# Kernel optimization log

Hardware: AMD Instinct MI355X
Metric: run time of the kernel (lower is better)

The kernel has to match this reference:

```python
import jax, jax.numpy as jnp
import numpy as np

B, N, DIM, H, DH = 32, 1024, 512, 8, 64
SCALE = DH ** -0.5


def setup_inputs() -> dict:
    key = jax.random.key(0)
    k1, k2, k3, k4 = jax.random.split(key, 4)
    x = jax.random.normal(k1, (B, N, DIM), dtype=jnp.float32)
    W_qkv = jax.random.normal(k2, (DIM, 3 * H * DH), dtype=jnp.float32) * (DIM ** -0.5)
    W_out = jax.random.normal(k3, (H * DH, DIM), dtype=jnp.float32) * ((H * DH) ** -0.5)
    b_out = jnp.zeros((DIM,), dtype=jnp.float32)
    decay_mask = jax.random.uniform(k4, (1, H, N, N), dtype=jnp.float32)
    return {"x": x, "W_qkv": W_qkv, "W_out": W_out, "b_out": b_out,
            "decay_mask": decay_mask}


def reference(x, W_qkv, W_out, b_out, decay_mask):
    b, n, _ = x.shape
    qkv = x @ W_qkv                                  # [b, n, 3*h*d]
    q, k, v = jnp.split(qkv, 3, axis=-1)
    reshape = lambda t: t.reshape(b, n, H, DH).transpose(0, 2, 1, 3)  # b h n d
    q, k, v = reshape(q), reshape(k), reshape(v)
    dots = jnp.einsum('bhid,bhjd->bhij', q, k) * SCALE
    attn = jax.nn.softmax(dots, axis=-1)
    attn = attn * decay_mask                          # post-softmax decay mask
    out = jnp.einsum('bhij,bhjd->bhid', attn, v)      # [b, h, n, d]
    out = out.transpose(0, 2, 1, 3).reshape(b, n, H * DH)
    return out @ W_out + b_out
```

## Files before the change

kernel.cpp:

```cpp
#include <hip/hip_runtime.h>
#include <hip/hip_fp16.h>
#include <math.h>

#define Bb 32
#define Nn 1024
#define DIMc 512
#define Hh 8
#define DHd 64
#define GK 512

typedef __attribute__((ext_vector_type(8))) short short8;
typedef __attribute__((ext_vector_type(8))) _Float16 half8;
typedef __attribute__((ext_vector_type(2))) __fp16 fp16x2;
typedef __attribute__((ext_vector_type(4))) float floatx4;

#define MFMA16 __builtin_amdgcn_mfma_f32_16x16x32_f16

#if __has_builtin(__builtin_amdgcn_exp2f)
#define EXP2(x) __builtin_amdgcn_exp2f(x)
#else
#define EXP2(x) __expf((x) * 0.6931471805599453f)
#endif

__device__ __forceinline__ unsigned short f16_bits(float f) {
    return __half_as_ushort(__float2half(f));
}
__device__ __forceinline__ int cvt_pk_f16(float a, float b) {
    fp16x2 r = __builtin_amdgcn_cvt_pkrtz(a, b);
    return __builtin_bit_cast(int, r);
}

__global__ __launch_bounds__(256) void transpose_half_kernel(
    const float* __restrict__ src, int K, int N,
    unsigned short* __restrict__ dh)
{
    __shared__ float T[32][33];
    const int tid = threadIdx.x;
    const int c = tid & 31, r0 = tid >> 5;
    const int nb = blockIdx.x * 32, kb = blockIdx.y * 32;
    #pragma unroll
    for (int i = 0; i < 4; ++i)
        T[r0 + i * 8][c] = src[(size_t)(kb + r0 + i * 8) * N + nb + c];
    __syncthreads();
    #pragma unroll
    for (int i = 0; i < 4; ++i) {
        int n = r0 + i * 8;
        dh[(size_t)(nb + n) * K + kb + c] = f16_bits(T[c][n]);
    }
}

__global__ __launch_bounds__(256) void decay_to_half_kernel(
    const float* __restrict__ D, unsigned short* __restrict__ D16)
{
    size_t i = ((size_t)blockIdx.x * 256 + threadIdx.x) * 4;
    float4 v = *(const float4*)(D + i);
    ushort4 o;
    o.x = f16_bits(v.x * 0.00390625f);
    o.y = f16_bits(v.y * 0.00390625f);
    o.z = f16_bits(v.z * 0.00390625f);
    o.w = f16_bits(v.w * 0.00390625f);
    *(ushort4*)(D16 + i) = o;
}

__global__ __launch_bounds__(256) void x_to_half_kernel(
    const float* __restrict__ X, unsigned short* __restrict__ Xf)
{
    size_t i = ((size_t)blockIdx.x * 256 + threadIdx.x) * 8;
    float4 a = *(const float4*)(X + i);
    float4 b = *(const float4*)(X + i + 4);
    float f[8] = {a.x, a.y, a.z, a.w, b.x, b.y, b.z, b.w};
    short8 o;
    #pragma unroll
    for (int e = 0; e < 8; ++e) o[e] = (short)f16_bits(f[e]);
    *(short8*)(Xf + i) = o;
}

__device__ __forceinline__ void gload_lds16(const unsigned short* g, unsigned short* l) {
    __builtin_amdgcn_global_load_lds(
        (const __attribute__((address_space(1))) unsigned int*)g,
        (__attribute__((address_space(3))) unsigned int*)l,
        16, 0, 0);
}

__global__ __launch_bounds__(256) void gemm_qkv_mfma(
    const unsigned short* __restrict__ Xf, const unsigned short* __restrict__ Wf,
    unsigned short* __restrict__ Qf, unsigned short* __restrict__ Kf,
    unsigned short* __restrict__ Vt)
{
    __shared__ union {
        struct { unsigned short Af[2][4096], Bf[2][4096]; } s;
        unsigned short bounce[128][136];
    } u;

    const int tid  = threadIdx.x;
    const int w    = tid >> 6;
    const int lane = tid & 63;
    const int quad = lane >> 4;
    const int l16  = lane & 15;
    const int lb = blockIdx.x;
    const int wg = (lb & 7) * 384 + (lb >> 3);
    const int n0 = (wg % 12) * 128;
    const int m0 = (wg / 12) * 128;
    const int wm = w >> 1, wn = w & 1;

    floatx4 acc[4][4];
    #pragma unroll
    for (int im = 0; im < 4; ++im)
        #pragma unroll
        for (int in = 0; in < 4; ++in)
            acc[im][in] = (floatx4){0.f, 0.f, 0.f, 0.f};

    #pragma unroll
    for (int i = 0; i < 2; ++i) {
        const int row = i * 64 + w * 16 + l16;
        const size_t aoff = (size_t)(m0 + row) * GK + quad * 8;
        const size_t boff = (size_t)(n0 + row) * GK + quad * 8;
        const int lbe = (i * 4 + w) * 512;
        gload_lds16(Xf + aoff, &u.s.Af[0][lbe]);
        gload_lds16(Wf + boff, &u.s.Bf[0][lbe]);
    }

    int cur = 0;
    for (int k0 = 0; k0 < GK; k0 += 32) {
        __syncthreads();
        if (k0 + 32 < GK) {
            const int kn = k0 + 32;
            #pragma unroll
            for (int i = 0; i < 2; ++i) {
                const int row = i * 64 + w * 16 + l16;
                const size_t aoff = (size_t)(m0 + row) * GK + kn + quad * 8;
                const size_t boff = (size_t)(n0 + row) * GK + kn + quad * 8;
                const int lbe = (i * 4 + w) * 512;
                gload_lds16(Xf + aoff, &u.s.Af[cur ^ 1][lbe]);
                gload_lds16(Wf + boff, &u.s.Bf[cur ^ 1][lbe]);
            }
        }

        half8 faf[4], fbf[4];
        #pragma unroll
        for (int t = 0; t < 4; ++t) {
            const int ca = ((wm * 4 + t) * 4 + quad) * 16 + l16;
            faf[t] = *(const half8*)&u.s.Af[cur][ca * 8];
            const int cb = ((wn * 4 + t) * 4 + quad) * 16 + l16;
            fbf[t] = *(const half8*)&u.s.Bf[cur][cb * 8];
        }
        #pragma unroll
        for (int im = 0; im < 4; ++im)
            #pragma unroll
            for (int in = 0; in < 4; ++in)
                acc[im][in] = MFMA16(faf[im], fbf[in], acc[im][in], 0, 0, 0);
        cur ^= 1;
    }

    const int which = n0 >> 9;
    const int b    = m0 >> 10;
    const int tokb = m0 & 1023;
    if (which < 2) {
        unsigned short* OUT = which ? Kf : Qf;
        const float sc = which ? 1.0f : 0.18033688011112042f;
        #pragma unroll
        for (int im = 0; im < 4; ++im) {
            const int tok = tokb + wm * 64 + im * 16 + quad * 4;
            #pragma unroll
            for (int in = 0; in < 4; ++in) {
                const int ncol = n0 + wn * 64 + in * 16 + l16;
                const int h = (ncol & 511) >> 6, d = ncol & 63;
                const size_t base = ((size_t)(b * Hh + h) * Nn + tok) * DHd + d;
                #pragma unroll
                for (int r = 0; r < 4; ++r)
                    OUT[base + (size_t)r * DHd] = f16_bits(acc[im][in][r] * sc);
            }
        }
    } else {
        __syncthreads();
        #pragma unroll
        for (int im = 0; im < 4; ++im)
            #pragma unroll
            for (int in = 0; in < 4; ++in)
                #pragma unroll
                for (int r = 0; r < 4; ++r)
                    u.bounce[wm * 64 + im * 16 + quad * 4 + r][wn * 64 + in * 16 + l16] =
                        f16_bits(acc[im][in][r]);
        __syncthreads();
        const int c = tid >> 1, tq = (tid & 1) * 64;
        const int h = ((n0 + c) & 511) >> 6, d = c & 63;
        unsigned short* vbase = Vt + ((size_t)(b * Hh + h) * DHd + d) * Nn + tokb;
        #pragma unroll
        for (int uu = 0; uu < 8; ++uu) {
            short8 v8;
            #pragma unroll
            for (int e = 0; e < 8; ++e)
                v8[e] = (short)u.bounce[tq + uu * 8 + e][c];
            *(short8*)&vbase[tq + uu * 8] = v8;
        }
    }
}

__global__ __launch_bounds__(256) void attn_mfma_kernel(
    const unsigned short* __restrict__ Qf, const unsigned short* __restrict__ Kf,
    const unsigned short* __restrict__ Vt, const unsigned short* __restrict__ D16,
    unsigned short* __restrict__ AOf)
{
    __shared__ unsigned short Kfs[2][32][72];
    __shared__ unsigned short Vts[2][64][40];

    const int tid  = threadIdx.x;
    const int wave = tid >> 6;
    const int lane = tid & 63;
    const int quad = lane >> 4;
    const int l16  = lane & 15;
    const int lb   = blockIdx.x;
    const int xcd  = lb & 7;
    const int r_   = lb >> 3;
    const int h    = r_ >> 5;
    const int rem  = r_ & 31;
    const int i0   = (rem >> 2) << 7;
    const int b    = xcd * 4 + (rem & 3);
    const int bh   = b * 8 + h;
    const int iw   = i0 + wave * 32;

    const size_t qoffA = ((size_t)bh * Nn + iw + l16) * DHd + quad * 8;
    const size_t qoffB = qoffA + (size_t)16 * DHd;
    const half8 qA0 = *(const half8*)(Qf + qoffA);
    const half8 qA1 = *(const half8*)(Qf + qoffA + 32);
    const half8 qB0 = *(const half8*)(Qf + qoffB);
    const half8 qB1 = *(const half8*)(Qf + qoffB + 32);

    floatx4 oA[4], oB[4];
    #pragma unroll
    for (int nt = 0; nt < 4; ++nt) {
        oA[nt] = (floatx4){0.f, 0.f, 0.f, 0.f};
        oB[nt] = (floatx4){0.f, 0.f, 0.f, 0.f};
    }
    float lA = 0.f, lB = 0.f;

    const int sj  = tid >> 3, sc2 = (tid & 7) * 8;
    const int prow = ((sj >> 2) & 1) * 16 + ((sj >> 3) << 2) + (sj & 3);
    const int vd  = tid >> 2, vj8 = (tid & 3) * 8;
    const unsigned short* DpA = D16 + ((size_t)h * Nn + iw + l16) * Nn + quad * 8;
    const unsigned short* DpB = DpA + (size_t)16 * Nn;

    const unsigned short* kpf = Kf + (size_t)bh * Nn * DHd + (size_t)sj * DHd + sc2;
    const unsigned short* vpv = Vt + (size_t)bh * DHd * Nn + (size_t)vd * Nn + vj8;

    short8 pk_f = *(const short8*)kpf; kpf += 32 * DHd;
    short8 pk_v = *(const short8*)vpv; vpv += 32;
    *(short8*)&Kfs[0][prow][sc2] = pk_f;
    *(short8*)&Vts[0][vd][vj8]   = pk_v;
    __syncthreads();

    int cur = 0;
    for (int j0 = 0; j0 < Nn; j0 += 32) {
        pk_f = *(const short8*)kpf; kpf += 32 * DHd;
        pk_v = *(const short8*)vpv; vpv += 32;
        const short8 dcA = *(const short8*)(DpA + j0);
        const short8 dcB = *(const short8*)(DpB + j0);

        floatx4 sA[2], sB[2];
        #pragma unroll
        for (int nh = 0; nh < 2; ++nh) {
            const int kr = nh * 16 + l16;
            half8 kf0 = *(const half8*)&Kfs[cur][kr][quad * 8];
            half8 kf1 = *(const half8*)&Kfs[cur][kr][32 + quad * 8];
            floatx4 a = (floatx4){0.f, 0.f, 0.f, 0.f};
            a = MFMA16(kf0, qA0, a, 0, 0, 0);
            a = MFMA16(kf1, qA1, a, 0, 0, 0);
            sA[nh] = a;
            floatx4 c = (floatx4){0.f, 0.f, 0.f, 0.f};
            c = MFMA16(kf0, qB0, c, 0, 0, 0);
            c = MFMA16(kf1, qB1, c, 0, 0, 0);
            sB[nh] = c;
        }

        float pA[8], pB[8];
        #pragma unroll
        for (int e = 0; e < 4; ++e) {
            pA[e]     = EXP2(sA[0][e]);
            pA[4 + e] = EXP2(sA[1][e]);
            pB[e]     = EXP2(sB[0][e]);
            pB[4 + e] = EXP2(sB[1][e]);
        }
        lA += ((pA[0] + pA[1]) + (pA[2] + pA[3])) + ((pA[4] + pA[5]) + (pA[6] + pA[7]));
        lB += ((pB[0] + pB[1]) + (pB[2] + pB[3])) + ((pB[4] + pB[5]) + (pB[6] + pB[7]));

        union { int i4[4]; half8 v8; } pfA, pfB;
        const int* dA = (const int*)&dcA;
        const int* dB = (const int*)&dcB;
        #pragma unroll
        for (int e = 0; e < 4; ++e) {
            fp16x2 pa = __builtin_bit_cast(fp16x2, cvt_pk_f16(pA[2 * e], pA[2 * e + 1]));
            fp16x2 da = __builtin_bit_cast(fp16x2, dA[e]);
            pfA.i4[e] = __builtin_bit_cast(int, pa * da);
            fp16x2 pb = __builtin_bit_cast(fp16x2, cvt_pk_f16(pB[2 * e], pB[2 * e + 1]));
            fp16x2 db = __builtin_bit_cast(fp16x2, dB[e]);
            pfB.i4[e] = __builtin_bit_cast(int, pb * db);
        }
        #pragma unroll
        for (int nt = 0; nt < 4; ++nt) {
            half8 vf = *(const half8*)&Vts[cur][nt * 16 + l16][quad * 8];
            oA[nt] = MFMA16(pfA.v8, vf, oA[nt], 0, 0, 0);
            oB[nt] = MFMA16(pfB.v8, vf, oB[nt], 0, 0, 0);
        }

        *(short8*)&Kfs[cur ^ 1][prow][sc2] = pk_f;
        *(short8*)&Vts[cur ^ 1][vd][vj8]   = pk_v;
        __syncthreads();
        cur ^= 1;
    }

    float lsA = lA;
    lsA += __shfl_xor(lsA, 16);
    lsA += __shfl_xor(lsA, 32);
    float lsB = lB;
    lsB += __shfl_xor(lsB, 16);
    lsB += __shfl_xor(lsB, 32);
    const float invA = 256.f / lsA;
    const float invB = 256.f / lsB;
    float irA[4], irB[4];
    #pragma unroll
    for (int r = 0; r < 4; ++r) {
        irA[r] = __shfl(invA, quad * 4 + r);
        irB[r] = __shfl(invB, quad * 4 + r);
    }
    const size_t aobA = ((size_t)b * Nn + iw) * DIMc + h * DHd;
    const size_t aobB = aobA + (size_t)16 * DIMc;
    #pragma unroll
    for (int nt = 0; nt < 4; ++nt)
        #pragma unroll
        for (int r = 0; r < 4; ++r) {
            const size_t ro = (size_t)(quad * 4 + r) * DIMc + nt * 16 + l16;
            AOf[aobA + ro] = f16_bits(oA[nt][r] * irA[r]);
            AOf[aobB + ro] = f16_bits(oB[nt][r] * irB[r]);
        }
}

__global__ __launch_bounds__(256) void gemm_out_mfma(
    const unsigned short* __restrict__ Af, const unsigned short* __restrict__ Wf,
    const float* __restrict__ bias, float* __restrict__ C)
{
    __shared__ struct { unsigned short Aa[2][4096], Bf[2][4096]; } s;

    const int tid  = threadIdx.x;
    const int w    = tid >> 6;
    const int lane = tid & 63;
    const int quad = lane >> 4;
    const int l16  = lane & 15;
    const int lb = blockIdx.x;
    const int wg = (lb & 7) * 128 + (lb >> 3);
    const int n0 = (wg & 3) * 128;
    const int m0 = (wg >> 2) * 128;
    const int wm = w >> 1, wn = w & 1;

    floatx4 acc[4][4];
    #pragma unroll
    for (int im = 0; im < 4; ++im)
        #pragma unroll
        for (int in = 0; in < 4; ++in)
            acc[im][in] = (floatx4){0.f, 0.f, 0.f, 0.f};

    #pragma unroll
    for (int i = 0; i < 2; ++i) {
        const int row = i * 64 + w * 16 + l16;
        const size_t aoff = (size_t)(m0 + row) * GK + quad * 8;
        const size_t boff = (size_t)(n0 + row) * GK + quad * 8;
        const int lbe = (i * 4 + w) * 512;
        gload_lds16(Af + aoff, &s.Aa[0][lbe]);
        gload_lds16(Wf + boff, &s.Bf[0][lbe]);
    }

    int cur = 0;
    for (int k0 = 0; k0 < GK; k0 += 32) {
        __syncthreads();
        if (k0 + 32 < GK) {
            const int kn = k0 + 32;
            #pragma unroll
            for (int i = 0; i < 2; ++i) {
                const int row = i * 64 + w * 16 + l16;
                const size_t aoff = (size_t)(m0 + row) * GK + kn + quad * 8;
                const size_t boff = (size_t)(n0 + row) * GK + kn + quad * 8;
                const int lbe = (i * 4 + w) * 512;
                gload_lds16(Af + aoff, &s.Aa[cur ^ 1][lbe]);
                gload_lds16(Wf + boff, &s.Bf[cur ^ 1][lbe]);
            }
        }

        half8 faf[4], fbf[4];
        #pragma unroll
        for (int t = 0; t < 4; ++t) {
            const int ca = ((wm * 4 + t) * 4 + quad) * 16 + l16;
            faf[t] = *(const half8*)&s.Aa[cur][ca * 8];
            const int cb = ((wn * 4 + t) * 4 + quad) * 16 + l16;
            fbf[t] = *(const half8*)&s.Bf[cur][cb * 8];
        }
        #pragma unroll
        for (int im = 0; im < 4; ++im)
            #pragma unroll
            for (int in = 0; in < 4; ++in)
                acc[im][in] = MFMA16(faf[im], fbf[in], acc[im][in], 0, 0, 0);
        cur ^= 1;
    }

    float biasv[4];
    #pragma unroll
    for (int in = 0; in < 4; ++in) biasv[in] = bias[n0 + wn * 64 + in * 16 + l16];
    #pragma unroll
    for (int im = 0; im < 4; ++im)
        #pragma unroll
        for (int in = 0; in < 4; ++in) {
            const int mrow = m0 + wm * 64 + im * 16 + quad * 4;
            const int ncol = n0 + wn * 64 + in * 16 + l16;
            #pragma unroll
            for (int r = 0; r < 4; ++r)
                C[(size_t)(mrow + r) * DIMc + ncol] = acc[im][in][r] + biasv[in];
        }
}

extern "C" void kernel_launch(void* const* d_in, const int* in_sizes, int n_in,
                              void* d_out, int out_size, void* d_ws, size_t ws_size,
                              hipStream_t stream)
{
    const float* x     = (const float*)d_in[0];
    const float* Wqkv  = (const float*)d_in[1];
    const float* Wout  = (const float*)d_in[2];
    const float* bout  = (const float*)d_in[3];
    const float* decay = (const float*)d_in[4];

    const size_t E = (size_t)32768 * 512;
    unsigned short* p = (unsigned short*)d_ws;
    unsigned short* Qf  = p; p += E;
    unsigned short* Kf  = p; p += E;
    unsigned short* Vt  = p; p += E;
    unsigned short* AOf = p; p += E;
    unsigned short* Wq  = p; p += 786432;
    unsigned short* Wo  = p; p += 262144;
    unsigned short* D16 = p;
    unsigned short* Xf = AOf;

    transpose_half_kernel<<<dim3(48, 16), 256, 0, stream>>>(Wqkv, 512, 1536, Wq);
    transpose_half_kernel<<<dim3(16, 16), 256, 0, stream>>>(Wout, 512, 512, Wo);
    decay_to_half_kernel<<<dim3(8192), 256, 0, stream>>>(decay, D16);
    x_to_half_kernel<<<dim3(8192), 256, 0, stream>>>(x, Xf);
    gemm_qkv_mfma<<<dim3(3072), 256, 0, stream>>>(Xf, Wq, Qf, Kf, Vt);
    attn_mfma_kernel<<<dim3(2048), 256, 0, stream>>>(Qf, Kf, Vt, D16, AOf);
    gemm_out_mfma<<<dim3(1024), 256, 0, stream>>>(AOf, Wo, bout, (float*)d_out);
}
```

Before: 288.1 us.

## Triple-buffer LDS staging in QKV and output GEMMs with explicit waitcnt

Both MFMA GEMM kernels now use three LDS stages instead of two and prefetch two k-tiles ahead. A manual `s_waitcnt vmcnt(4)` plus a raw barrier replaces `__syncthreads`, so the loads for the next tile stay in flight while the current tile is computed. The aim is to hide global-to-LDS latency better in the projection GEMMs. The cost is LDS rising from 32 KB to 48 KB per block, which can lower occupancy. The last iterations also issue unguarded prefetches past the K extent; their buffers are never read, but the final rows may read slightly beyond the array.

```diff
diff --git a/kernel.cpp b/kernel.cpp
--- a/kernel.cpp
+++ b/kernel.cpp
@@ -82,13 +82,25 @@
         16, 0, 0);
 }
 
+#define STAGE2(PA, PB, k0s, bufp) do {                                         \
+    _Pragma("unroll")                                                          \
+    for (int i_ = 0; i_ < 2; ++i_) {                                           \
+        const int row_ = i_ * 64 + w * 16 + l16;                               \
+        const size_t aoff_ = (size_t)(m0 + row_) * GK + (k0s) + quad * 8;      \
+        const size_t boff_ = (size_t)(n0 + row_) * GK + (k0s) + quad * 8;      \
+        const int lbe_ = (i_ * 4 + w) * 512;                                   \
+        gload_lds16((PA) + aoff_, (bufp) + lbe_);                              \
+        gload_lds16((PB) + boff_, (bufp) + 4096 + lbe_);                       \
+    }                                                                          \
+} while (0)
+
 __global__ __launch_bounds__(256) void gemm_qkv_mfma(
     const unsigned short* __restrict__ Xf, const unsigned short* __restrict__ Wf,
     unsigned short* __restrict__ Qf, unsigned short* __restrict__ Kf,
     unsigned short* __restrict__ Vt)
 {
     __shared__ union {
-        struct { unsigned short Af[2][4096], Bf[2][4096]; } s;
+        unsigned short buf[3][8192];
         unsigned short bounce[128][136];
     } u;
 
@@ -110,47 +122,34 @@
         for (int in = 0; in < 4; ++in)
             acc[im][in] = (floatx4){0.f, 0.f, 0.f, 0.f};
 
-    #pragma unroll
-    for (int i = 0; i < 2; ++i) {
-        const int row = i * 64 + w * 16 + l16;
-        const size_t aoff = (size_t)(m0 + row) * GK + quad * 8;
-        const size_t boff = (size_t)(n0 + row) * GK + quad * 8;
-        const int lbe = (i * 4 + w) * 512;
-        gload_lds16(Xf + aoff, &u.s.Af[0][lbe]);
-        gload_lds16(Wf + boff, &u.s.Bf[0][lbe]);
-    }
-
-    int cur = 0;
+    STAGE2(Xf, Wf, 0, u.buf[0]);
+    STAGE2(Xf, Wf, 32, u.buf[1]);
+
+    int rd = 0;
     for (int k0 = 0; k0 < GK; k0 += 32) {
-        __syncthreads();
-        if (k0 + 32 < GK) {
-            const int kn = k0 + 32;
-            #pragma unroll
-            for (int i = 0; i < 2; ++i) {
-                const int row = i * 64 + w * 16 + l16;
-                const size_t aoff = (size_t)(m0 + row) * GK + kn + quad * 8;
-                const size_t boff = (size_t)(n0 + row) * GK + kn + quad * 8;
-                const int lbe = (i * 4 + w) * 512;
-                gload_lds16(Xf + aoff, &u.s.Af[cur ^ 1][lbe]);
-                gload_lds16(Wf + boff, &u.s.Bf[cur ^ 1][lbe]);
-            }
-        }
-
+        asm volatile("s_waitcnt vmcnt(4) lgkmcnt(0)" ::: "memory");
+        __builtin_amdgcn_s_barrier();
+        __builtin_amdgcn_sched_barrier(0);
+        const int wr = (rd >= 1) ? rd - 1 : 2;
+        STAGE2(Xf, Wf, k0 + 64, u.buf[wr]);
+
+        const unsigned short* rp = u.buf[rd];
         half8 faf[4], fbf[4];
         #pragma unroll
         for (int t = 0; t < 4; ++t) {
             const int ca = ((wm * 4 + t) * 4 + quad) * 16 + l16;
-            faf[t] = *(const half8*)&u.s.Af[cur][ca * 8];
+            faf[t] = *(const half8*)&rp[ca * 8];
             const int cb = ((wn * 4 + t) * 4 + quad) * 16 + l16;
-            fbf[t] = *(const half8*)&u.s.Bf[cur][cb * 8];
+            fbf[t] = *(const half8*)&rp[4096 + cb * 8];
         }
         #pragma unroll
         for (int im = 0; im < 4; ++im)
             #pragma unroll
             for (int in = 0; in < 4; ++in)
                 acc[im][in] = MFMA16(faf[im], fbf[in], acc[im][in], 0, 0, 0);
-        cur ^= 1;
-    }
+        rd = (rd == 2) ? 0 : rd + 1;
+    }
+    asm volatile("s_waitcnt vmcnt(0)" ::: "memory");
 
     const int which = n0 >> 9;
     const int b    = m0 >> 10;
@@ -338,7 +337,7 @@
     const unsigned short* __restrict__ Af, const unsigned short* __restrict__ Wf,
     const float* __restrict__ bias, float* __restrict__ C)
 {
-    __shared__ struct { unsigned short Aa[2][4096], Bf[2][4096]; } s;
+    __shared__ unsigned short sbuf[3][8192];
 
     const int tid  = threadIdx.x;
     const int w    = tid >> 6;
@@ -358,47 +357,34 @@
         for (int in = 0; in < 4; ++in)
             acc[im][in] = (floatx4){0.f, 0.f, 0.f, 0.f};
 
-    #pragma unroll
-    for (int i = 0; i < 2; ++i) {
-        const int row = i * 64 + w * 16 + l16;
-        const size_t aoff = (size_t)(m0 + row) * GK + quad * 8;
-        const size_t boff = (size_t)(n0 + row) * GK + quad * 8;
-        const int lbe = (i * 4 + w) * 512;
-        gload_lds16(Af + aoff, &s.Aa[0][lbe]);
-        gload_lds16(Wf + boff, &s.Bf[0][lbe]);
-    }
-
-    int cur = 0;
+    STAGE2(Af, Wf, 0, sbuf[0]);
+    STAGE2(Af, Wf, 32, sbuf[1]);
+
+    int rd = 0;
     for (int k0 = 0; k0 < GK; k0 += 32) {
-        __syncthreads();
-        if (k0 + 32 < GK) {
-            const int kn = k0 + 32;
-            #pragma unroll
-            for (int i = 0; i < 2; ++i) {
-                const int row = i * 64 + w * 16 + l16;
-                const size_t aoff = (size_t)(m0 + row) * GK + kn + quad * 8;
-                const size_t boff = (size_t)(n0 + row) * GK + kn + quad * 8;
-                const int lbe = (i * 4 + w) * 512;
-                gload_lds16(Af + aoff, &s.Aa[cur ^ 1][lbe]);
-                gload_lds16(Wf + boff, &s.Bf[cur ^ 1][lbe]);
-            }
-        }
-
+        asm volatile("s_waitcnt vmcnt(4) lgkmcnt(0)" ::: "memory");
+        __builtin_amdgcn_s_barrier();
+        __builtin_amdgcn_sched_barrier(0);
+        const int wr = (rd >= 1) ? rd - 1 : 2;
+        STAGE2(Af, Wf, k0 + 64, sbuf[wr]);
+
+        const unsigned short* rp = sbuf[rd];
         half8 faf[4], fbf[4];
         #pragma unroll
         for (int t = 0; t < 4; ++t) {
             const int ca = ((wm * 4 + t) * 4 + quad) * 16 + l16;
-            faf[t] = *(const half8*)&s.Aa[cur][ca * 8];
+            faf[t] = *(const half8*)&rp[ca * 8];
             const int cb = ((wn * 4 + t) * 4 + quad) * 16 + l16;
-            fbf[t] = *(const half8*)&s.Bf[cur][cb * 8];
+            fbf[t] = *(const half8*)&rp[4096 + cb * 8];
         }
         #pragma unroll
         for (int im = 0; im < 4; ++im)
             #pragma unroll
             for (int in = 0; in < 4; ++in)
                 acc[im][in] = MFMA16(faf[im], fbf[in], acc[im][in], 0, 0, 0);
-        cur ^= 1;
-    }
+        rd = (rd == 2) ? 0 : rd + 1;
+    }
+    asm volatile("s_waitcnt vmcnt(0)" ::: "memory");
 
     float biasv[4];
     #pragma unroll
```

Result: no change. 293.7 us (+1.9%).
